# Performance work log

Measured on AMD Instinct MI355X. Metric: run time of the kernel, lower is better.

The kernel has to match this reference:

```python
import jax, jax.numpy as jnp
import numpy as np

TEMP_DIV = 13.0  # forward hard-codes attn / 13 (self.temperature is unused)


def setup_inputs() -> dict:
    key = jax.random.key(0)
    k1, k2, k3 = jax.random.split(key, 3)
    B, Lq, Lk, D = 8, 2048, 2048, 640
    q = jax.random.normal(k1, (B, Lq, D), dtype=jnp.float32)
    k = jax.random.normal(k2, (B, Lk, D), dtype=jnp.float32)
    v = jax.random.normal(k3, (B, Lk, D), dtype=jnp.float32)
    return {"q": q, "k": k, "v": v}


def _l2_scores(q, k):
    # -sum((q[:,:,None,:] - k[:,None,:,:])**2, axis=3) via the GEMM expansion
    # ||q||^2 - 2 q.k + ||k||^2  -> avoids the (B,Lq,Lk,D) intermediate.
    qq = jnp.sum(q * q, axis=-1)            # (B, Lq)
    kk = jnp.sum(k * k, axis=-1)            # (B, Lk)
    qk = jnp.einsum('bqd,bkd->bqk', q, k)   # (B, Lq, Lk)
    return -(qq[:, :, None] - 2.0 * qk + kk[:, None, :])


def reference(q, k, v):
    attn_logits = _l2_scores(q, k) / TEMP_DIV          # (B, Lq, Lk)
    log_attn = jax.nn.log_softmax(attn_logits, axis=2)
    attn = jnp.exp(log_attn)                            # softmax, shares the stable pass
    # dropout is identity in eval mode
    output = jnp.einsum('bqk,bkd->bqd', attn, v)        # bmm
    return (output, attn, log_attn)
```

## Files before the change

kernel.cpp:

```cpp
#include <hip/hip_runtime.h>


#define B_   8
#define LQ   2048
#define LK   2048
#define DD   640

typedef short s16x8 __attribute__((ext_vector_type(8)));
typedef float f32x4 __attribute__((ext_vector_type(4)));

__device__ __forceinline__ unsigned short f2bf(float x) {
    unsigned int u = __float_as_uint(x);
    unsigned int r = (u + 0x7fffu + ((u >> 16) & 1u)) >> 16;
    return (unsigned short)r;
}

__global__ __launch_bounds__(256) void cvt_norm(const float* __restrict__ src,
                                                unsigned short* __restrict__ dst,
                                                float* __restrict__ nrm) {
    int row  = blockIdx.x * 4 + (threadIdx.x >> 6);
    int lane = threadIdx.x & 63;
    const float4* s = (const float4*)(src + (size_t)row * DD);
    unsigned short* d = dst + (size_t)row * DD;
    float ss = 0.f;
    for (int t = lane; t < DD / 4; t += 64) {
        float4 x = s[t];
        ss += x.x * x.x + x.y * x.y + x.z * x.z + x.w * x.w;
        ushort4 o;
        o.x = f2bf(x.x); o.y = f2bf(x.y); o.z = f2bf(x.z); o.w = f2bf(x.w);
        *(ushort4*)(d + t * 4) = o;
    }
    #pragma unroll
    for (int o = 32; o; o >>= 1) ss += __shfl_xor(ss, o);
    if (lane == 0) nrm[row] = ss;
}

__global__ __launch_bounds__(256) void cvt_transpose_v(const float* __restrict__ v,
                                                       unsigned short* __restrict__ vt) {
    __shared__ float tile[64][65];
    int bx = blockIdx.x;
    int b  = bx / 320;
    int r  = bx % 320;
    int tj = r / 10;
    int td = r % 10;
    const float* src = v + (size_t)b * LK * DD + (size_t)tj * 64 * DD + td * 64;
    for (int e = threadIdx.x; e < 4096; e += 256) {
        int rr = e >> 6, cc = e & 63;
        tile[rr][cc] = src[(size_t)rr * DD + cc];
    }
    __syncthreads();
    unsigned short* dst = vt + (size_t)b * DD * LK + (size_t)td * 64 * LK + tj * 64;
    for (int e = threadIdx.x; e < 4096; e += 256) {
        int rr = e >> 6, cc = e & 63;
        dst[(size_t)rr * LK + cc] = f2bf(tile[cc][rr]);
    }
}

template <int LDAB, int KSZ, int NTN, bool EPI>
__global__ __launch_bounds__(256) void gemm_nt(
    const unsigned short* __restrict__ A, const unsigned short* __restrict__ Bm,
    float* __restrict__ C, size_t strideA, size_t strideB, size_t strideC, int ldc,
    const float* __restrict__ qq, const float* __restrict__ kkn) {
    __shared__ unsigned short lA[128 * 64];
    __shared__ unsigned short lB[128 * 64];
    __shared__ float snm[256];

    int bx = blockIdx.x;
    int b  = bx / (16 * NTN);
    int r  = bx % (16 * NTN);
    int tm = r / NTN, tn = r % NTN;

    const unsigned short* Ab = A + b * strideA + (size_t)tm * 128 * LDAB;
    const unsigned short* Bb = Bm + b * strideB + (size_t)tn * 128 * LDAB;

    int tid = threadIdx.x;
    int wave = tid >> 6, lane = tid & 63;

    if (EPI) {
        if (tid < 128) snm[tid] = qq[b * LQ + tm * 128 + tid];
        else           snm[tid] = kkn[b * LK + tn * 128 + (tid - 128)];
    }

    f32x4 acc[4][4] = {};
    int wm = wave >> 1, wn = wave & 1;
    int lrow = lane & 15;
    int lk8  = (lane >> 4) * 8;
    int srow = lane >> 3;
    int scol = (lane & 7) * 8;

    for (int k0 = 0; k0 < KSZ; k0 += 64) {
        __syncthreads();
        #pragma unroll
        for (int c = 0; c < 4; ++c) {
            int rbase = (c * 4 + wave) * 8;
            __builtin_amdgcn_global_load_lds(
                (const __attribute__((address_space(1))) void*)(Ab + (size_t)(rbase + srow) * LDAB + k0 + scol),
                (__attribute__((address_space(3))) void*)(lA + rbase * 64), 16, 0, 0);
            __builtin_amdgcn_global_load_lds(
                (const __attribute__((address_space(1))) void*)(Bb + (size_t)(rbase + srow) * LDAB + k0 + scol),
                (__attribute__((address_space(3))) void*)(lB + rbase * 64), 16, 0, 0);
        }
        __syncthreads();
        #pragma unroll
        for (int kk = 0; kk < 64; kk += 32) {
            s16x8 af[4], bf[4];
            #pragma unroll
            for (int t = 0; t < 4; ++t)
                af[t] = *(const s16x8*)(lA + (wm * 64 + t * 16 + lrow) * 64 + kk + lk8);
            #pragma unroll
            for (int t = 0; t < 4; ++t)
                bf[t] = *(const s16x8*)(lB + (wn * 64 + t * 16 + lrow) * 64 + kk + lk8);
            #pragma unroll
            for (int mt = 0; mt < 4; ++mt)
                #pragma unroll
                for (int nt = 0; nt < 4; ++nt)
                    acc[mt][nt] = __builtin_amdgcn_mfma_f32_16x16x32_bf16(
                        af[mt], bf[nt], acc[mt][nt], 0, 0, 0);
        }
    }

    float* Cb = C + b * strideC + (size_t)(tm * 128) * ldc + tn * 128;
    #pragma unroll
    for (int mt = 0; mt < 4; ++mt)
        #pragma unroll
        for (int nt = 0; nt < 4; ++nt) {
            int col = wn * 64 + nt * 16 + lrow;
            int rb  = wm * 64 + mt * 16 + ((lane >> 4) << 2);
            #pragma unroll
            for (int rr = 0; rr < 4; ++rr) {
                float val = acc[mt][nt][rr];
                if (EPI) val = (2.0f * val - snm[rb + rr] - snm[128 + col]) * (1.0f / 13.0f);
                Cb[(size_t)(rb + rr) * ldc + col] = val;
            }
        }
}

__global__ __launch_bounds__(256) void softmax_fix(float* __restrict__ logits,
                                                   float* __restrict__ attn,
                                                   unsigned short* __restrict__ a16) {
    __shared__ float redm[4], reds[4];
    size_t row = blockIdx.x;
    float* Lr = logits + row * LK;
    int tid = threadIdx.x;
    float x[8];
    *(float4*)(x)     = *(const float4*)(Lr + tid * 8);
    *(float4*)(x + 4) = *(const float4*)(Lr + tid * 8 + 4);

    float m = x[0];
    #pragma unroll
    for (int i = 1; i < 8; ++i) m = fmaxf(m, x[i]);
    #pragma unroll
    for (int o = 32; o; o >>= 1) m = fmaxf(m, __shfl_xor(m, o));
    int wv = tid >> 6, ln = tid & 63;
    if (ln == 0) redm[wv] = m;
    __syncthreads();
    m = fmaxf(fmaxf(redm[0], redm[1]), fmaxf(redm[2], redm[3]));

    float e[8];
    float s = 0.f;
    #pragma unroll
    for (int i = 0; i < 8; ++i) { e[i] = __expf(x[i] - m); s += e[i]; }
    #pragma unroll
    for (int o = 32; o; o >>= 1) s += __shfl_xor(s, o);
    if (ln == 0) reds[wv] = s;
    __syncthreads();
    s = reds[0] + reds[1] + reds[2] + reds[3];

    float lse = __logf(s);
    float inv = 1.0f / s;
    float at[8], la[8];
    #pragma unroll
    for (int i = 0; i < 8; ++i) { at[i] = e[i] * inv; la[i] = x[i] - m - lse; }

    float* Ar = attn + row * LK;
    *(float4*)(Ar + tid * 8)     = *(float4*)at;
    *(float4*)(Ar + tid * 8 + 4) = *(float4*)(at + 4);
    *(float4*)(Lr + tid * 8)     = *(float4*)la;
    *(float4*)(Lr + tid * 8 + 4) = *(float4*)(la + 4);

    unsigned short h[8];
    #pragma unroll
    for (int i = 0; i < 8; ++i) h[i] = f2bf(at[i]);
    unsigned short* Hr = a16 + row * LK;
    *(ushort4*)(Hr + tid * 8)     = *(ushort4*)h;
    *(ushort4*)(Hr + tid * 8 + 4) = *(ushort4*)(h + 4);
}

extern "C" void kernel_launch(void* const* d_in, const int* in_sizes, int n_in,
                              void* d_out, int out_size, void* d_ws, size_t ws_size,
                              hipStream_t stream) {
    const float* q = (const float*)d_in[0];
    const float* k = (const float*)d_in[1];
    const float* v = (const float*)d_in[2];

    float* out   = (float*)d_out;
    float* attn  = out + (size_t)B_ * LQ * DD;
    float* logat = attn + (size_t)B_ * LQ * LK;

    unsigned short* q16  = (unsigned short*)d_ws;
    unsigned short* k16  = q16 + (size_t)B_ * LQ * DD;
    unsigned short* v16t = k16 + (size_t)B_ * LK * DD;
    unsigned short* a16  = v16t + (size_t)B_ * DD * LK;
    float* qq  = (float*)(a16 + (size_t)B_ * LQ * LK);
    float* kkn = qq + (size_t)B_ * LQ;

    cvt_norm<<<B_ * LQ / 4, 256, 0, stream>>>(q, q16, qq);
    cvt_norm<<<B_ * LK / 4, 256, 0, stream>>>(k, k16, kkn);
    cvt_transpose_v<<<B_ * (LK / 64) * (DD / 64), 256, 0, stream>>>(v, v16t);

    gemm_nt<DD, DD, 16, true><<<B_ * 16 * 16, 256, 0, stream>>>(
        q16, k16, logat,
        (size_t)LQ * DD, (size_t)LK * DD, (size_t)LQ * LK, LK, qq, kkn);

    softmax_fix<<<B_ * LQ, 256, 0, stream>>>(logat, attn, a16);

    gemm_nt<LK, LK, 5, false><<<B_ * 16 * 5, 256, 0, stream>>>(
        a16, v16t, out,
        (size_t)LQ * LK, (size_t)DD * LK, (size_t)LQ * DD, DD, nullptr, nullptr);
}
```

Before: 628.1 us.

## Fuse q/k conversion launches and remap GEMM block order for XCD-local reuse

Merges the two bf16 conversion and norm kernels for q and k into a single launch, saving one kernel launch. Also remaps the GEMM block index so that the low three bits (likely the XCD under round-robin dispatch) select a pair of M-tiles. Consecutive blocks on one XCD then share the same A row-tiles and step across N tiles, which is meant to improve L2 reuse. The remapping depends on how blocks are dispatched across XCDs and may not help if that assumption is wrong.

```diff
diff --git a/kernel.cpp b/kernel.cpp
--- a/kernel.cpp
+++ b/kernel.cpp
@@ -15,13 +15,22 @@
     return (unsigned short)r;
 }
 
-__global__ __launch_bounds__(256) void cvt_norm(const float* __restrict__ src,
-                                                unsigned short* __restrict__ dst,
-                                                float* __restrict__ nrm) {
+__global__ __launch_bounds__(256) void cvt_norm2(const float* __restrict__ q,
+                                                 const float* __restrict__ k,
+                                                 unsigned short* __restrict__ q16,
+                                                 unsigned short* __restrict__ k16,
+                                                 float* __restrict__ qq,
+                                                 float* __restrict__ kkn) {
     int row  = blockIdx.x * 4 + (threadIdx.x >> 6);
     int lane = threadIdx.x & 63;
-    const float4* s = (const float4*)(src + (size_t)row * DD);
-    unsigned short* d = dst + (size_t)row * DD;
+    const float* src;
+    unsigned short* dst;
+    float* nrm;
+    int r;
+    if (row < B_ * LQ) { src = q; dst = q16; nrm = qq;  r = row; }
+    else               { src = k; dst = k16; nrm = kkn; r = row - B_ * LQ; }
+    const float4* s = (const float4*)(src + (size_t)r * DD);
+    unsigned short* d = dst + (size_t)r * DD;
     float ss = 0.f;
     for (int t = lane; t < DD / 4; t += 64) {
         float4 x = s[t];
@@ -32,7 +41,7 @@
     }
     #pragma unroll
     for (int o = 32; o; o >>= 1) ss += __shfl_xor(ss, o);
-    if (lane == 0) nrm[row] = ss;
+    if (lane == 0) nrm[r] = ss;
 }
 
 __global__ __launch_bounds__(256) void cvt_transpose_v(const float* __restrict__ v,
@@ -65,10 +74,14 @@
     __shared__ unsigned short lB[128 * 64];
     __shared__ float snm[256];
 
+    constexpr int G = NTN * 2;
     int bx = blockIdx.x;
-    int b  = bx / (16 * NTN);
-    int r  = bx % (16 * NTN);
-    int tm = r / NTN, tn = r % NTN;
+    int x  = bx & 7;
+    int i  = bx >> 3;
+    int b  = i / G;
+    int j  = i % G;
+    int tn = j >> 1;
+    int tm = (x << 1) | (j & 1);
 
     const unsigned short* Ab = A + b * strideA + (size_t)tm * 128 * LDAB;
     const unsigned short* Bb = Bm + b * strideB + (size_t)tn * 128 * LDAB;
@@ -204,8 +217,7 @@
     float* qq  = (float*)(a16 + (size_t)B_ * LQ * LK);
     float* kkn = qq + (size_t)B_ * LQ;
 
-    cvt_norm<<<B_ * LQ / 4, 256, 0, stream>>>(q, q16, qq);
-    cvt_norm<<<B_ * LK / 4, 256, 0, stream>>>(k, k16, kkn);
+    cvt_norm2<<<2 * B_ * LQ / 4, 256, 0, stream>>>(q, k, q16, k16, qq, kkn);
     cvt_transpose_v<<<B_ * (LK / 64) * (DD / 64), 256, 0, stream>>>(v, v16t);
 
     gemm_nt<DD, DD, 16, true><<<B_ * 16 * 16, 256, 0, stream>>>(
```

New measurement: 625.1 us. Within noise of the previous version (-0.5%).
